# Optimization experiments

Measured on AMD Instinct MI355X. Metric: run time of the kernel, lower is better.

## Reference

```python
import jax, jax.numpy as jnp
import numpy as np

ENC_DIM = 512
QUERY_DIM = 1024
ATTN_DIM = 128
CONV_CH = 32
KERNEL = 31
B, T = 64, 2048


def setup_inputs() -> dict:
    key = jax.random.key(0)
    ks = jax.random.split(key, 9)
    s = 0.02
    encoder_outputs = jax.random.normal(ks[0], (B, T, ENC_DIM), dtype=jnp.float32)
    decoder_hidden = jax.random.normal(ks[1], (B, QUERY_DIM), dtype=jnp.float32)
    prev_attention = jax.random.uniform(ks[2], (B, T), dtype=jnp.float32)
    prev_attention = prev_attention / jnp.sum(prev_attention, axis=1, keepdims=True)
    Wq = jax.random.normal(ks[3], (QUERY_DIM, ATTN_DIM), dtype=jnp.float32) * s
    Wk = jax.random.normal(ks[4], (ENC_DIM, ATTN_DIM), dtype=jnp.float32) * s
    conv_w = jax.random.normal(ks[5], (CONV_CH, 1, KERNEL), dtype=jnp.float32) * s  # OIH
    conv_b = jax.random.normal(ks[6], (CONV_CH,), dtype=jnp.float32) * s
    Wloc = jax.random.normal(ks[7], (CONV_CH, ATTN_DIM), dtype=jnp.float32) * s
    v = jax.random.normal(ks[8], (ATTN_DIM,), dtype=jnp.float32) * s
    return {"encoder_outputs": encoder_outputs, "decoder_hidden": decoder_hidden,
            "prev_attention": prev_attention, "Wq": Wq, "Wk": Wk,
            "conv_w": conv_w, "conv_b": conv_b, "Wloc": Wloc, "v": v}


def reference(encoder_outputs, decoder_hidden, prev_attention, Wq, Wk, conv_w, conv_b, Wloc, v):
    # query: [B, 1, A]
    query = (decoder_hidden @ Wq)[:, None, :]
    # keys: [B, T, A]
    keys = jnp.einsum('bte,ea->bta', encoder_outputs, Wk)
    # location conv: prev_attention [B, T] -> [B, 1, T] -> [B, C, T], SAME padding
    pad = (KERNEL - 1) // 2
    loc = jax.lax.conv_general_dilated(
        prev_attention[:, None, :], conv_w,
        window_strides=(1,), padding=[(pad, pad)],
        dimension_numbers=('NCH', 'OIH', 'NCH'))
    loc = loc + conv_b[None, :, None]
    # [B, T, C] -> [B, T, A]
    location_term = jnp.einsum('bct,ca->bta', loc, Wloc)
    energy = jnp.einsum('bta,a->bt', jnp.tanh(keys + query + location_term), v)
    return jax.nn.softmax(energy, axis=1)
```

## Files before the change

### kernel.cpp

```cpp
#include <hip/hip_runtime.h>
#include <hip/hip_bf16.h>

#define B_  64
#define T_  2048
#define E_  512
#define Q_  1024
#define A_  128
#define C_  32
#define KW_ 31

using bf16x8 = __attribute__((ext_vector_type(8))) short;
using f32x4  = __attribute__((ext_vector_type(4))) float;

__device__ __forceinline__ short f2bf(float f) {
  union { float f; unsigned u; } x; x.f = f;
  unsigned r = x.u + 0x7fffu + ((x.u >> 16) & 1u);
  return (short)(r >> 16);
}

__device__ __forceinline__ bf16x8 pack8(float4 a, float4 b) {
  union { bf16x8 v; __hip_bfloat162 h[4]; } u;
  u.h[0] = __float22bfloat162_rn(make_float2(a.x, a.y));
  u.h[1] = __float22bfloat162_rn(make_float2(a.z, a.w));
  u.h[2] = __float22bfloat162_rn(make_float2(b.x, b.y));
  u.h[3] = __float22bfloat162_rn(make_float2(b.z, b.w));
  return u.v;
}

__device__ __forceinline__ float fast_tanh(float x) {
  float e2 = __expf(2.f * x);
  return 1.f - 2.f * __builtin_amdgcn_rcpf(e2 + 1.f);
}

__device__ __forceinline__ void gload16(const void* g, void* l) {
  __builtin_amdgcn_global_load_lds(
      (const __attribute__((address_space(1))) unsigned int*)g,
      (__attribute__((address_space(3))) unsigned int*)l, 16, 0, 0);
}

__global__ __launch_bounds__(256) void prep_kernel(
    const float* __restrict__ dh, const float* __restrict__ Wq,
    const float* __restrict__ conv_b, const float* __restrict__ Wloc,
    const float* __restrict__ Wk,
    unsigned short* __restrict__ wkf, unsigned short* __restrict__ wlocf,
    float* __restrict__ q2p)
{
  int blk = blockIdx.x;
  int tid = threadIdx.x;
  if (blk < 512) {
    __shared__ float part[128];
    int b = blk >> 3, kq = blk & 7;
    int a = tid & 127, kh = tid >> 7;
    const float* dhr = dh + b * Q_ + kq * 128 + kh * 64;
    const float* wq  = Wq + (size_t)(kq * 128 + kh * 64) * A_ + a;
    float s = 0.f;
    #pragma unroll 8
    for (int k = 0; k < 64; ++k) s += dhr[k] * wq[(size_t)k * A_];
    if (kh) part[a] = s;
    __syncthreads();
    if (!kh) {
      s += part[a];
      if (kq == 0) {
        float t = 0.f;
        #pragma unroll 8
        for (int c = 0; c < C_; ++c) t += conv_b[c] * Wloc[c * A_ + a];
        s += t;
      }
      q2p[(kq * B_ + b) * A_ + a] = s;
    }
  } else if (blk < 544) {
    int wave = tid >> 6, lane = tid & 63;
    int g = (blk - 512) * 4 + wave;
    int ks = g >> 3, nt = g & 7;
    int lg = lane >> 4, lr = lane & 15;
    bf16x8 o;
    #pragma unroll
    for (int j = 0; j < 8; ++j)
      o[j] = f2bf(Wk[(ks * 32 + lg * 8 + j) * A_ + nt * 16 + lr]);
    *(bf16x8*)(wkf + ((size_t)g * 64 + lane) * 8) = o;
  } else {
    int wave = tid >> 6, lane = tid & 63;
    int g = (blk - 544) * 4 + wave;
    int lg = lane >> 4, lr = lane & 15;
    bf16x8 o;
    #pragma unroll
    for (int j = 0; j < 8; ++j)
      o[j] = f2bf(Wloc[(lg * 8 + j) * A_ + g * 16 + lr]);
    *(bf16x8*)(wlocf + ((size_t)g * 64 + lane) * 8) = o;
  }
}

__global__ __launch_bounds__(512, 2) void energy_kernel(
    const float* __restrict__ enc, const float* __restrict__ prev,
    const float* __restrict__ conv_w,
    const unsigned short* __restrict__ wkfall,
    const float* __restrict__ q2p, const float* __restrict__ vvec,
    float* __restrict__ outexp, float* __restrict__ psum)
{
  __shared__ unsigned short sWB[69632];
  __shared__ float sprev[288];
  __shared__ float scw[KW_][C_];
  __shared__ float swsum[8];

  int tid = threadIdx.x;
  int wave = tid >> 6, lane = tid & 63;
  int lg = lane >> 4, lr = lane & 15;
  int m0 = blockIdx.x * 256;
  int b  = m0 >> 11, t0 = m0 & (T_ - 1);
  int wm = m0 + wave * 32;

  #pragma unroll
  for (int s = 0; s < 17; ++s)
    gload16(wkfall + (size_t)s * 4096 + wave * 512 + lane * 8,
            &sWB[s * 4096 + wave * 512]);

  for (int i = tid; i < 286; i += 512) {
    int t = t0 - 15 + i;
    sprev[i] = (t >= 0 && t < T_) ? prev[b * T_ + t] : 0.f;
  }
  for (int i = tid; i < KW_ * C_; i += 512)
    scw[i >> 5][i & 31] = conv_w[(i & 31) * KW_ + (i >> 5)];

  const float* encR0 = enc + (size_t)(wm + lr) * E_ + lg * 8;
  const float* encR1 = encR0 + 16 * E_;
  float4 pa0 = *(const float4*)(encR0),      pa1 = *(const float4*)(encR0 + 4);
  float4 pa2 = *(const float4*)(encR1),      pa3 = *(const float4*)(encR1 + 4);
  float4 pb0 = *(const float4*)(encR0 + 32), pb1 = *(const float4*)(encR0 + 36);
  float4 pb2 = *(const float4*)(encR1 + 32), pb3 = *(const float4*)(encR1 + 36);

  asm volatile("s_waitcnt lgkmcnt(0)" ::: "memory");
  __builtin_amdgcn_s_barrier();
  __builtin_amdgcn_sched_barrier(0);
  float c0[8], c1[8];
  #pragma unroll
  for (int c = 0; c < 8; ++c) { c0[c] = 0.f; c1[c] = 0.f; }
  {
    int r0 = wave * 32 + lr, r1 = r0 + 16;
    for (int j = 0; j < KW_; ++j) {
      float p0 = sprev[r0 + j], p1 = sprev[r1 + j];
      float4 wA = *(const float4*)&scw[j][lg * 8];
      float4 wB = *(const float4*)&scw[j][lg * 8 + 4];
      c0[0] += p0 * wA.x; c0[1] += p0 * wA.y; c0[2] += p0 * wA.z; c0[3] += p0 * wA.w;
      c0[4] += p0 * wB.x; c0[5] += p0 * wB.y; c0[6] += p0 * wB.z; c0[7] += p0 * wB.w;
      c1[0] += p1 * wA.x; c1[1] += p1 * wA.y; c1[2] += p1 * wA.z; c1[3] += p1 * wA.w;
      c1[4] += p1 * wB.x; c1[5] += p1 * wB.y; c1[6] += p1 * wB.z; c1[7] += p1 * wB.w;
    }
  }
  bf16x8 afl0 = pack8(make_float4(c0[0], c0[1], c0[2], c0[3]),
                      make_float4(c0[4], c0[5], c0[6], c0[7]));
  bf16x8 afl1 = pack8(make_float4(c1[0], c1[1], c1[2], c1[3]),
                      make_float4(c1[4], c1[5], c1[6], c1[7]));

  asm volatile("s_waitcnt vmcnt(16)" ::: "memory");
  __builtin_amdgcn_sched_barrier(0);
  __builtin_amdgcn_s_barrier();

  f32x4 acc0[8], acc1[8];
  {
    const unsigned short* base = &sWB[16 * 4096 + lane * 8];
    #pragma unroll
    for (int nt = 0; nt < 8; ++nt) {
      bf16x8 bfr = *(const bf16x8*)(base + nt * 512);
      acc0[nt] = __builtin_amdgcn_mfma_f32_16x16x32_bf16(afl0, bfr, (f32x4){0,0,0,0}, 0, 0, 0);
      acc1[nt] = __builtin_amdgcn_mfma_f32_16x16x32_bf16(afl1, bfr, (f32x4){0,0,0,0}, 0, 0, 0);
    }
  }

  #pragma unroll 1
  for (int i = 0; i < 8; ++i) {
    {
      bf16x8 af0 = pack8(pa0, pa1), af1 = pack8(pa2, pa3);
      if (i < 7) {
        const float* r0 = encR0 + (2 * i + 2) * 32;
        const float* r1 = encR1 + (2 * i + 2) * 32;
        pa0 = *(const float4*)(r0); pa1 = *(const float4*)(r0 + 4);
        pa2 = *(const float4*)(r1); pa3 = *(const float4*)(r1 + 4);
      }
      const unsigned short* base = &sWB[(2 * i) * 4096 + lane * 8];
      #pragma unroll
      for (int nt = 0; nt < 8; ++nt) {
        bf16x8 bfr = *(const bf16x8*)(base + nt * 512);
        acc0[nt] = __builtin_amdgcn_mfma_f32_16x16x32_bf16(af0, bfr, acc0[nt], 0, 0, 0);
        acc1[nt] = __builtin_amdgcn_mfma_f32_16x16x32_bf16(af1, bfr, acc1[nt], 0, 0, 0);
      }
    }
    {
      bf16x8 bg0 = pack8(pb0, pb1), bg1 = pack8(pb2, pb3);
      if (i < 7) {
        const float* r0 = encR0 + (2 * i + 3) * 32;
        const float* r1 = encR1 + (2 * i + 3) * 32;
        pb0 = *(const float4*)(r0); pb1 = *(const float4*)(r0 + 4);
        pb2 = *(const float4*)(r1); pb3 = *(const float4*)(r1 + 4);
      }
      const unsigned short* base = &sWB[(2 * i + 1) * 4096 + lane * 8];
      #pragma unroll
      for (int nt = 0; nt < 8; ++nt) {
        bf16x8 bfr = *(const bf16x8*)(base + nt * 512);
        acc0[nt] = __builtin_amdgcn_mfma_f32_16x16x32_bf16(bg0, bfr, acc0[nt], 0, 0, 0);
        acc1[nt] = __builtin_amdgcn_mfma_f32_16x16x32_bf16(bg1, bfr, acc1[nt], 0, 0, 0);
      }
    }
  }

  float qv[8], vv[8];
  #pragma unroll
  for (int nt = 0; nt < 8; ++nt) {
    int n = nt * 16 + lr;
    float s = 0.f;
    #pragma unroll
    for (int p = 0; p < 8; ++p) s += q2p[(p * B_ + b) * A_ + n];
    qv[nt] = s;
    vv[nt] = vvec[n];
  }
  float ssum = 0.f;
  #pragma unroll
  for (int f = 0; f < 2; ++f) {
    f32x4* acc = f ? acc1 : acc0;
    float p0 = 0, p1 = 0, p2 = 0, p3 = 0;
    #pragma unroll
    for (int nt = 0; nt < 8; ++nt) {
      p0 += fast_tanh(acc[nt][0] + qv[nt]) * vv[nt];
      p1 += fast_tanh(acc[nt][1] + qv[nt]) * vv[nt];
      p2 += fast_tanh(acc[nt][2] + qv[nt]) * vv[nt];
      p3 += fast_tanh(acc[nt][3] + qv[nt]) * vv[nt];
    }
    #pragma unroll
    for (int off = 1; off < 16; off <<= 1) {
      p0 += __shfl_xor(p0, off, 64);
      p1 += __shfl_xor(p1, off, 64);
      p2 += __shfl_xor(p2, off, 64);
      p3 += __shfl_xor(p3, off, 64);
    }
    float e0 = __expf(p0), e1 = __expf(p1), e2 = __expf(p2), e3 = __expf(p3);
    ssum += (e0 + e1) + (e2 + e3);
    if (lr == 0)
      *(float4*)(outexp + wm + f * 16 + lg * 4) = make_float4(e0, e1, e2, e3);
  }
  ssum += __shfl_xor(ssum, 16, 64);
  ssum += __shfl_xor(ssum, 32, 64);
  if (lane == 0) swsum[wave] = ssum;
  __syncthreads();
  if (tid == 0) {
    float s = 0.f;
    #pragma unroll
    for (int wv = 0; wv < 8; ++wv) s += swsum[wv];
    psum[b * 8 + (blockIdx.x & 7)] = s;
  }
}

__global__ __launch_bounds__(256) void norm_kernel(float* __restrict__ out,
                                                   const float* __restrict__ psum)
{
  int b = blockIdx.x, tid = threadIdx.x;
  float s = 0.f;
  #pragma unroll
  for (int p = 0; p < 8; ++p) s += psum[b * 8 + p];
  float inv = 1.f / s;
  float4* row = (float4*)(out + (size_t)b * T_);
  #pragma unroll
  for (int j = 0; j < 2; ++j) {
    float4 x = row[tid + j * 256];
    x.x *= inv; x.y *= inv; x.z *= inv; x.w *= inv;
    row[tid + j * 256] = x;
  }
}

extern "C" void kernel_launch(void* const* d_in, const int* in_sizes, int n_in,
                              void* d_out, int out_size, void* d_ws, size_t ws_size,
                              hipStream_t stream)
{
  const float* enc   = (const float*)d_in[0];
  const float* dh    = (const float*)d_in[1];
  const float* prev  = (const float*)d_in[2];
  const float* Wq    = (const float*)d_in[3];
  const float* Wk    = (const float*)d_in[4];
  const float* convw = (const float*)d_in[5];
  const float* convb = (const float*)d_in[6];
  const float* Wloc  = (const float*)d_in[7];
  const float* v     = (const float*)d_in[8];
  float* out = (float*)d_out;

  char* w = (char*)d_ws;
  unsigned short* wkf   = (unsigned short*)w;
  unsigned short* wlocf = (unsigned short*)(w + 131072);
  float*          q2p   = (float*)(w + 139264);
  float*          psum  = (float*)(w + 401408);

  hipLaunchKernelGGL(prep_kernel, dim3(546), dim3(256), 0, stream,
                     dh, Wq, convb, Wloc, Wk, wkf, wlocf, q2p);
  hipLaunchKernelGGL(energy_kernel, dim3(512), dim3(512), 0, stream,
                     enc, prev, convw, wkf, q2p, v, out, psum);
  hipLaunchKernelGGL(norm_kernel, dim3(64), dim3(256), 0, stream, out, psum);
}
```

Measured before the change: 68.76 us.

## Fold conv weights into Wloc and double rows per energy block

The location conv and Wloc projection are folded into one combined 31x128 matrix G in the prep kernel. The energy kernel then feeds shifted prev_attention windows straight into MFMA as the K=32 slice, which removes the per-block shared-memory conv. Each wave now handles 64 rows instead of 32, so the grid halves to 256 blocks and each shared-memory weight fragment is reused across four row groups. The cost is more register pressure from 32 accumulators and more in-flight loads, plus fewer blocks to cover the GPU.

```diff
diff --git a/kernel.cpp b/kernel.cpp
--- a/kernel.cpp
+++ b/kernel.cpp
@@ -41,9 +41,8 @@
 __global__ __launch_bounds__(256) void prep_kernel(
     const float* __restrict__ dh, const float* __restrict__ Wq,
     const float* __restrict__ conv_b, const float* __restrict__ Wloc,
-    const float* __restrict__ Wk,
-    unsigned short* __restrict__ wkf, unsigned short* __restrict__ wlocf,
-    float* __restrict__ q2p)
+    const float* __restrict__ Wk, const float* __restrict__ conv_w,
+    unsigned short* __restrict__ wkf, float* __restrict__ q2p)
 {
   int blk = blockIdx.x;
   int tid = threadIdx.x;
@@ -62,7 +61,6 @@
       s += part[a];
       if (kq == 0) {
         float t = 0.f;
-        #pragma unroll 8
         for (int c = 0; c < C_; ++c) t += conv_b[c] * Wloc[c * A_ + a];
         s += t;
       }
@@ -79,125 +77,143 @@
       o[j] = f2bf(Wk[(ks * 32 + lg * 8 + j) * A_ + nt * 16 + lr]);
     *(bf16x8*)(wkf + ((size_t)g * 64 + lane) * 8) = o;
   } else {
+    __shared__ float G[32][128];
+    for (int i = tid; i < 4096; i += 256) {
+      int j = i >> 7, a = i & 127;
+      float s = 0.f;
+      if (j < KW_)
+        for (int c = 0; c < C_; ++c) s += conv_w[c * KW_ + j] * Wloc[c * A_ + a];
+      G[j][a] = s;
+    }
+    __syncthreads();
     int wave = tid >> 6, lane = tid & 63;
-    int g = (blk - 544) * 4 + wave;
     int lg = lane >> 4, lr = lane & 15;
-    bf16x8 o;
-    #pragma unroll
-    for (int j = 0; j < 8; ++j)
-      o[j] = f2bf(Wloc[(lg * 8 + j) * A_ + g * 16 + lr]);
-    *(bf16x8*)(wlocf + ((size_t)g * 64 + lane) * 8) = o;
+    #pragma unroll
+    for (int h = 0; h < 2; ++h) {
+      int nt = wave * 2 + h;
+      bf16x8 o;
+      #pragma unroll
+      for (int j = 0; j < 8; ++j) o[j] = f2bf(G[lg * 8 + j][nt * 16 + lr]);
+      *(bf16x8*)(wkf + ((size_t)(128 + nt) * 64 + lane) * 8) = o;
+    }
   }
 }
 
 __global__ __launch_bounds__(512, 2) void energy_kernel(
     const float* __restrict__ enc, const float* __restrict__ prev,
-    const float* __restrict__ conv_w,
     const unsigned short* __restrict__ wkfall,
     const float* __restrict__ q2p, const float* __restrict__ vvec,
     float* __restrict__ outexp, float* __restrict__ psum)
 {
   __shared__ unsigned short sWB[69632];
-  __shared__ float sprev[288];
-  __shared__ float scw[KW_][C_];
   __shared__ float swsum[8];
 
   int tid = threadIdx.x;
   int wave = tid >> 6, lane = tid & 63;
   int lg = lane >> 4, lr = lane & 15;
-  int m0 = blockIdx.x * 256;
-  int b  = m0 >> 11, t0 = m0 & (T_ - 1);
-  int wm = m0 + wave * 32;
+  int m0 = blockIdx.x * 512;
+  int b  = m0 >> 11;
+  int wm = m0 + wave * 64;
 
   #pragma unroll
   for (int s = 0; s < 17; ++s)
     gload16(wkfall + (size_t)s * 4096 + wave * 512 + lane * 8,
             &sWB[s * 4096 + wave * 512]);
 
-  for (int i = tid; i < 286; i += 512) {
-    int t = t0 - 15 + i;
-    sprev[i] = (t >= 0 && t < T_) ? prev[b * T_ + t] : 0.f;
-  }
-  for (int i = tid; i < KW_ * C_; i += 512)
-    scw[i >> 5][i & 31] = conv_w[(i & 31) * KW_ + (i >> 5)];
-
-  const float* encR0 = enc + (size_t)(wm + lr) * E_ + lg * 8;
-  const float* encR1 = encR0 + 16 * E_;
-  float4 pa0 = *(const float4*)(encR0),      pa1 = *(const float4*)(encR0 + 4);
-  float4 pa2 = *(const float4*)(encR1),      pa3 = *(const float4*)(encR1 + 4);
-  float4 pb0 = *(const float4*)(encR0 + 32), pb1 = *(const float4*)(encR0 + 36);
-  float4 pb2 = *(const float4*)(encR1 + 32), pb3 = *(const float4*)(encR1 + 36);
-
-  asm volatile("s_waitcnt lgkmcnt(0)" ::: "memory");
-  __builtin_amdgcn_s_barrier();
-  __builtin_amdgcn_sched_barrier(0);
-  float c0[8], c1[8];
-  #pragma unroll
-  for (int c = 0; c < 8; ++c) { c0[c] = 0.f; c1[c] = 0.f; }
-  {
-    int r0 = wave * 32 + lr, r1 = r0 + 16;
-    for (int j = 0; j < KW_; ++j) {
-      float p0 = sprev[r0 + j], p1 = sprev[r1 + j];
-      float4 wA = *(const float4*)&scw[j][lg * 8];
-      float4 wB = *(const float4*)&scw[j][lg * 8 + 4];
-      c0[0] += p0 * wA.x; c0[1] += p0 * wA.y; c0[2] += p0 * wA.z; c0[3] += p0 * wA.w;
-      c0[4] += p0 * wB.x; c0[5] += p0 * wB.y; c0[6] += p0 * wB.z; c0[7] += p0 * wB.w;
-      c1[0] += p1 * wA.x; c1[1] += p1 * wA.y; c1[2] += p1 * wA.z; c1[3] += p1 * wA.w;
-      c1[4] += p1 * wB.x; c1[5] += p1 * wB.y; c1[6] += p1 * wB.z; c1[7] += p1 * wB.w;
-    }
-  }
-  bf16x8 afl0 = pack8(make_float4(c0[0], c0[1], c0[2], c0[3]),
-                      make_float4(c0[4], c0[5], c0[6], c0[7]));
-  bf16x8 afl1 = pack8(make_float4(c1[0], c1[1], c1[2], c1[3]),
-                      make_float4(c1[4], c1[5], c1[6], c1[7]));
-
-  asm volatile("s_waitcnt vmcnt(16)" ::: "memory");
+  const float* prevb = prev + b * T_;
+  int tl = (m0 & (T_ - 1)) + wave * 64 + lr;
+  float pv[32];
+  #pragma unroll
+  for (int g = 0; g < 4; ++g) {
+    #pragma unroll
+    for (int j = 0; j < 8; ++j) {
+      int u = tl + 16 * g - 15 + lg * 8 + j;
+      int uc = min(max(u, 0), T_ - 1);
+      pv[g * 8 + j] = prevb[uc];
+    }
+  }
+
+  const float* eR = enc + (size_t)(wm + lr) * E_ + lg * 8;
+  float4 sA[8], sB[8];
+  #pragma unroll
+  for (int g = 0; g < 4; ++g) {
+    const float* rg = eR + (size_t)g * 16 * E_;
+    sA[2 * g]     = *(const float4*)(rg);
+    sA[2 * g + 1] = *(const float4*)(rg + 4);
+    sB[2 * g]     = *(const float4*)(rg + 32);
+    sB[2 * g + 1] = *(const float4*)(rg + 36);
+  }
+
+  asm volatile("s_waitcnt vmcnt(0)" ::: "memory");
   __builtin_amdgcn_sched_barrier(0);
   __builtin_amdgcn_s_barrier();
 
-  f32x4 acc0[8], acc1[8];
+  f32x4 acc[4][8];
   {
+    bf16x8 ap[4];
+    #pragma unroll
+    for (int g = 0; g < 4; ++g) {
+      float m[8];
+      #pragma unroll
+      for (int j = 0; j < 8; ++j) {
+        int u = tl + 16 * g - 15 + lg * 8 + j;
+        m[j] = ((unsigned)u < (unsigned)T_) ? pv[g * 8 + j] : 0.f;
+      }
+      ap[g] = pack8(make_float4(m[0], m[1], m[2], m[3]),
+                    make_float4(m[4], m[5], m[6], m[7]));
+    }
     const unsigned short* base = &sWB[16 * 4096 + lane * 8];
     #pragma unroll
     for (int nt = 0; nt < 8; ++nt) {
       bf16x8 bfr = *(const bf16x8*)(base + nt * 512);
-      acc0[nt] = __builtin_amdgcn_mfma_f32_16x16x32_bf16(afl0, bfr, (f32x4){0,0,0,0}, 0, 0, 0);
-      acc1[nt] = __builtin_amdgcn_mfma_f32_16x16x32_bf16(afl1, bfr, (f32x4){0,0,0,0}, 0, 0, 0);
+      #pragma unroll
+      for (int g = 0; g < 4; ++g)
+        acc[g][nt] = __builtin_amdgcn_mfma_f32_16x16x32_bf16(ap[g], bfr, (f32x4){0,0,0,0}, 0, 0, 0);
     }
   }
 
   #pragma unroll 1
   for (int i = 0; i < 8; ++i) {
     {
-      bf16x8 af0 = pack8(pa0, pa1), af1 = pack8(pa2, pa3);
+      bf16x8 af[4];
+      #pragma unroll
+      for (int g = 0; g < 4; ++g) af[g] = pack8(sA[2 * g], sA[2 * g + 1]);
       if (i < 7) {
-        const float* r0 = encR0 + (2 * i + 2) * 32;
-        const float* r1 = encR1 + (2 * i + 2) * 32;
-        pa0 = *(const float4*)(r0); pa1 = *(const float4*)(r0 + 4);
-        pa2 = *(const float4*)(r1); pa3 = *(const float4*)(r1 + 4);
+        #pragma unroll
+        for (int g = 0; g < 4; ++g) {
+          const float* rg = eR + (size_t)g * 16 * E_ + (2 * i + 2) * 32;
+          sA[2 * g]     = *(const float4*)(rg);
+          sA[2 * g + 1] = *(const float4*)(rg + 4);
+        }
       }
       const unsigned short* base = &sWB[(2 * i) * 4096 + lane * 8];
       #pragma unroll
       for (int nt = 0; nt < 8; ++nt) {
         bf16x8 bfr = *(const bf16x8*)(base + nt * 512);
-        acc0[nt] = __builtin_amdgcn_mfma_f32_16x16x32_bf16(af0, bfr, acc0[nt], 0, 0, 0);
-        acc1[nt] = __builtin_amdgcn_mfma_f32_16x16x32_bf16(af1, bfr, acc1[nt], 0, 0, 0);
+        #pragma unroll
+        for (int g = 0; g < 4; ++g)
+          acc[g][nt] = __builtin_amdgcn_mfma_f32_16x16x32_bf16(af[g], bfr, acc[g][nt], 0, 0, 0);
       }
     }
     {
-      bf16x8 bg0 = pack8(pb0, pb1), bg1 = pack8(pb2, pb3);
+      bf16x8 af[4];
+      #pragma unroll
+      for (int g = 0; g < 4; ++g) af[g] = pack8(sB[2 * g], sB[2 * g + 1]);
       if (i < 7) {
-        const float* r0 = encR0 + (2 * i + 3) * 32;
-        const float* r1 = encR1 + (2 * i + 3) * 32;
-        pb0 = *(const float4*)(r0); pb1 = *(const float4*)(r0 + 4);
-        pb2 = *(const float4*)(r1); pb3 = *(const float4*)(r1 + 4);
+        #pragma unroll
+        for (int g = 0; g < 4; ++g) {
+          const float* rg = eR + (size_t)g * 16 * E_ + (2 * i + 3) * 32;
+          sB[2 * g]     = *(const float4*)(rg);
+          sB[2 * g + 1] = *(const float4*)(rg + 4);
+        }
       }
       const unsigned short* base = &sWB[(2 * i + 1) * 4096 + lane * 8];
       #pragma unroll
       for (int nt = 0; nt < 8; ++nt) {
         bf16x8 bfr = *(const bf16x8*)(base + nt * 512);
-        acc0[nt] = __builtin_amdgcn_mfma_f32_16x16x32_bf16(bg0, bfr, acc0[nt], 0, 0, 0);
-        acc1[nt] = __builtin_amdgcn_mfma_f32_16x16x32_bf16(bg1, bfr, acc1[nt], 0, 0, 0);
+        #pragma unroll
+        for (int g = 0; g < 4; ++g)
+          acc[g][nt] = __builtin_amdgcn_mfma_f32_16x16x32_bf16(af[g], bfr, acc[g][nt], 0, 0, 0);
       }
     }
   }
@@ -214,15 +230,14 @@
   }
   float ssum = 0.f;
   #pragma unroll
-  for (int f = 0; f < 2; ++f) {
-    f32x4* acc = f ? acc1 : acc0;
+  for (int g = 0; g < 4; ++g) {
     float p0 = 0, p1 = 0, p2 = 0, p3 = 0;
     #pragma unroll
     for (int nt = 0; nt < 8; ++nt) {
-      p0 += fast_tanh(acc[nt][0] + qv[nt]) * vv[nt];
-      p1 += fast_tanh(acc[nt][1] + qv[nt]) * vv[nt];
-      p2 += fast_tanh(acc[nt][2] + qv[nt]) * vv[nt];
-      p3 += fast_tanh(acc[nt][3] + qv[nt]) * vv[nt];
+      p0 += fast_tanh(acc[g][nt][0] + qv[nt]) * vv[nt];
+      p1 += fast_tanh(acc[g][nt][1] + qv[nt]) * vv[nt];
+      p2 += fast_tanh(acc[g][nt][2] + qv[nt]) * vv[nt];
+      p3 += fast_tanh(acc[g][nt][3] + qv[nt]) * vv[nt];
     }
     #pragma unroll
     for (int off = 1; off < 16; off <<= 1) {
@@ -234,7 +249,7 @@
     float e0 = __expf(p0), e1 = __expf(p1), e2 = __expf(p2), e3 = __expf(p3);
     ssum += (e0 + e1) + (e2 + e3);
     if (lr == 0)
-      *(float4*)(outexp + wm + f * 16 + lg * 4) = make_float4(e0, e1, e2, e3);
+      *(float4*)(outexp + wm + g * 16 + lg * 4) = make_float4(e0, e1, e2, e3);
   }
   ssum += __shfl_xor(ssum, 16, 64);
   ssum += __shfl_xor(ssum, 32, 64);
@@ -244,7 +259,7 @@
     float s = 0.f;
     #pragma unroll
     for (int wv = 0; wv < 8; ++wv) s += swsum[wv];
-    psum[b * 8 + (blockIdx.x & 7)] = s;
+    psum[b * 4 + (blockIdx.x & 3)] = s;
   }
 }
 
@@ -254,7 +269,7 @@
   int b = blockIdx.x, tid = threadIdx.x;
   float s = 0.f;
   #pragma unroll
-  for (int p = 0; p < 8; ++p) s += psum[b * 8 + p];
+  for (int p = 0; p < 4; ++p) s += psum[b * 4 + p];
   float inv = 1.f / s;
   float4* row = (float4*)(out + (size_t)b * T_);
   #pragma unroll
@@ -281,14 +296,13 @@
   float* out = (float*)d_out;
 
   char* w = (char*)d_ws;
-  unsigned short* wkf   = (unsigned short*)w;
-  unsigned short* wlocf = (unsigned short*)(w + 131072);
-  float*          q2p   = (float*)(w + 139264);
-  float*          psum  = (float*)(w + 401408);
-
-  hipLaunchKernelGGL(prep_kernel, dim3(546), dim3(256), 0, stream,
-                     dh, Wq, convb, Wloc, Wk, wkf, wlocf, q2p);
-  hipLaunchKernelGGL(energy_kernel, dim3(512), dim3(512), 0, stream,
-                     enc, prev, convw, wkf, q2p, v, out, psum);
+  unsigned short* wkf  = (unsigned short*)w;
+  float*          q2p  = (float*)(w + 139264);
+  float*          psum = (float*)(w + 401408);
+
+  hipLaunchKernelGGL(prep_kernel, dim3(545), dim3(256), 0, stream,
+                     dh, Wq, convb, Wloc, Wk, convw, wkf, q2p);
+  hipLaunchKernelGGL(energy_kernel, dim3(256), dim3(512), 0, stream,
+                     enc, prev, wkf, q2p, v, out, psum);
   hipLaunchKernelGGL(norm_kernel, dim3(64), dim3(256), 0, stream, out, psum);
 }
```

Measured after the change: 69.71 us. No clear change (+1.4%).
